# Kernel optimization log

Measured on AMD Instinct MI355X. Metric: run time of the kernel, lower is better.

Reference implementation:

```python
import jax, jax.numpy as jnp
import numpy as np

NUM_USERS = 1_000_000
NUM_AGES = 8
NUM_ATTR = 40
FACE_K = 64
VISUAL_DIM = 2048
HIDDEN = 512
BATCH = 16384
VOCAB = NUM_USERS + 24 + 2 + NUM_AGES + NUM_ATTR  # fm_linear input width


def setup_inputs() -> dict:
    key = jax.random.key(0)
    ks = jax.random.split(key, 24)
    s = 0.02
    inp = {
        "user_id": jax.random.randint(ks[0], (BATCH,), 0, NUM_USERS),
        "hour": jax.random.randint(ks[1], (BATCH,), 0, 24),
        "visual": jax.random.normal(ks[2], (BATCH, VISUAL_DIM), jnp.float32),
        "scale": jax.random.uniform(ks[3], (BATCH, 1), jnp.float32),
        "gender": jax.random.randint(ks[4], (BATCH,), 0, 2),
        "age": jax.random.randint(ks[5], (BATCH,), 0, NUM_AGES),
        "attribute": jax.random.randint(ks[6], (BATCH,), 0, NUM_ATTR),
        # embedding tables
        "user_emb": jax.random.normal(ks[7], (NUM_USERS, FACE_K), jnp.float32) * s,
        "hour_emb": jax.random.normal(ks[8], (24, FACE_K), jnp.float32) * s,
        "gender_emb": jax.random.normal(ks[9], (2, FACE_K), jnp.float32) * s,
        "age_emb": jax.random.normal(ks[10], (NUM_AGES, FACE_K), jnp.float32) * s,
        "attr_emb": jax.random.normal(ks[11], (NUM_ATTR, FACE_K), jnp.float32) * s,
        # visual linear
        "visu_w": jax.random.normal(ks[12], (FACE_K, VISUAL_DIM), jnp.float32) * s,
        "visu_b": jnp.zeros((FACE_K,), jnp.float32),
        # fm linear over concatenated one-hots (width VOCAB, out 2)
        "fm_w": jax.random.normal(ks[13], (2, VOCAB), jnp.float32) * s,
        "fm_b": jnp.zeros((2,), jnp.float32),
        # dnn
        "w1": jax.random.normal(ks[14], (HIDDEN, 6 * FACE_K), jnp.float32) * s,
        "b1": jnp.zeros((HIDDEN,), jnp.float32),
        "w2": jax.random.normal(ks[15], (HIDDEN, HIDDEN), jnp.float32) * s,
        "b2": jnp.zeros((HIDDEN,), jnp.float32),
        "w3": jax.random.normal(ks[16], (2, HIDDEN), jnp.float32) * s,
        "b3": jnp.zeros((2,), jnp.float32),
    }
    return inp


def reference(user_id, hour, visual, scale, gender, age, attribute,
              user_emb, hour_emb, gender_emb, age_emb, attr_emb,
              visu_w, visu_b, fm_w, fm_b, w1, b1, w2, b2, w3, b3):
    B = user_id.shape[0]
    # fm linear: one_hot @ W^T == gather-sum of W columns at the hot indices
    cols = jnp.stack([
        user_id,
        NUM_USERS + hour,
        NUM_USERS + 24 + gender,
        NUM_USERS + 24 + 2 + age,
        NUM_USERS + 24 + 2 + NUM_AGES + attribute,
    ], axis=1)  # [B, 5]
    linear_part = fm_w[:, cols].sum(axis=2).T + fm_b  # [B, 2]

    # embeddings
    user = user_emb[user_id]            # [B, K]
    hr = hour_emb[hour]                 # [B, K]
    face = jnp.stack([gender_emb[gender], attr_emb[attribute], age_emb[age]], axis=1)  # [B,3,K]
    face = scale[:, None, :] * jnp.tanh(face)  # scale [B,1] -> [B,1,1]
    embeddings = jnp.concatenate([user[:, None, :], hr[:, None, :], face], axis=1)  # [B,5,K]

    # FM second order
    so = jnp.square(embeddings.sum(axis=1)) - jnp.square(embeddings).sum(axis=1)  # [B,K]
    second_order = 0.5 * so.sum(axis=1)  # [B]
    fm = linear_part + second_order[:, None]  # [B,2]

    # DNN
    vis = visual @ visu_w.T + visu_b  # [B,K]
    x = jnp.concatenate([embeddings.reshape(B, 5 * FACE_K), vis], axis=1)  # [B,6K]
    x = jax.nn.relu(x @ w1.T + b1)
    x = jax.nn.relu(x @ w2.T + b2)
    x = x @ w3.T + b3
    return jax.nn.softmax(fm + x, axis=1)
```

## Files before the change

### kernel.cpp

```cpp
#include <hip/hip_runtime.h>
#include <hip/hip_bf16.h>
#include <stdint.h>

#define BATCH 16384
#define FACE_K 64
#define VISUAL_DIM 2048
#define HIDDEN 512
#define NUM_USERS 1000000
#define NUM_AGES 8
#define NUM_ATTR 40
#define VOCAB (NUM_USERS + 24 + 2 + NUM_AGES + NUM_ATTR)
#define XDIM 384
#define XS 388
#define HS 516

typedef __bf16 bf16x8 __attribute__((ext_vector_type(8)));
typedef float f32x4 __attribute__((ext_vector_type(4)));

__device__ __forceinline__ uint16_t f2bf(float f) {
    union { float f; uint32_t u; } v; v.f = f;
    uint32_t r = v.u + 0x7fffu + ((v.u >> 16) & 1u);
    return (uint16_t)(r >> 16);
}

__device__ __forceinline__ bf16x8 cvt8(float4 a, float4 b) {
    bf16x8 r;
    r[0] = (__bf16)a.x; r[1] = (__bf16)a.y; r[2] = (__bf16)a.z; r[3] = (__bf16)a.w;
    r[4] = (__bf16)b.x; r[5] = (__bf16)b.y; r[6] = (__bf16)b.z; r[7] = (__bf16)b.w;
    return r;
}

__global__ void cvt_frag(const float* __restrict__ visu_w, const float* __restrict__ w1,
                         const float* __restrict__ w2, uint16_t* __restrict__ vwb,
                         uint16_t* __restrict__ w1b, uint16_t* __restrict__ w2b) {
    int tid = blockIdx.x * blockDim.x + threadIdx.x;
    const float* src;
    uint16_t* dst;
    if (tid < 16384) {
        int lane = tid & 63, fi = tid >> 6;
        int lc = lane & 15, quad = lane >> 4;
        int j = fi & 3, kk = (fi >> 2) & 31, kh = fi >> 7;
        src = visu_w + (size_t)(j * 16 + lc) * VISUAL_DIM + kh * 1024 + kk * 32 + quad * 8;
        dst = vwb + (size_t)tid * 8;
    } else if (tid < 40960) {
        int t2 = tid - 16384;
        int lane = t2 & 63, fi = t2 >> 6;
        int lc = lane & 15, quad = lane >> 4;
        int j = fi & 7, csks = fi >> 3;
        int ks = csks % 12, cs = csks / 12;
        src = w1 + (size_t)(cs * 128 + j * 16 + lc) * XDIM + ks * 32 + quad * 8;
        dst = w1b + (size_t)t2 * 8;
    } else {
        int t3 = tid - 40960;
        int lane = t3 & 63, fi = t3 >> 6;
        int lc = lane & 15, quad = lane >> 4;
        int j = fi & 7, csks = fi >> 3;
        int ks = csks & 15, cs = csks >> 4;
        src = w2 + (size_t)(cs * 128 + j * 16 + lc) * HIDDEN + ks * 32 + quad * 8;
        dst = w2b + (size_t)t3 * 8;
    }
    float4 a = *(const float4*)src;
    float4 b = *(const float4*)(src + 4);
    ushort4 o0, o1;
    o0.x = f2bf(a.x); o0.y = f2bf(a.y); o0.z = f2bf(a.z); o0.w = f2bf(a.w);
    o1.x = f2bf(b.x); o1.y = f2bf(b.y); o1.z = f2bf(b.z); o1.w = f2bf(b.w);
    *(ushort4*)dst = o0;
    *(ushort4*)(dst + 4) = o1;
}

__global__ __launch_bounds__(256) void mega_kernel(
        const int* __restrict__ uid, const int* __restrict__ hour,
        const float* __restrict__ visual, const float* __restrict__ scale,
        const int* __restrict__ gender, const int* __restrict__ age,
        const int* __restrict__ attr,
        const float* __restrict__ user_emb, const float* __restrict__ hour_emb,
        const float* __restrict__ gender_emb, const float* __restrict__ age_emb,
        const float* __restrict__ attr_emb,
        const uint16_t* __restrict__ vwb, const float* __restrict__ visu_b,
        const float* __restrict__ fm_w, const float* __restrict__ fm_b,
        const uint16_t* __restrict__ w1b, const float* __restrict__ b1,
        const uint16_t* __restrict__ w2b, const float* __restrict__ b2,
        const float* __restrict__ w3, const float* __restrict__ b3,
        float* __restrict__ out) {
    __shared__ uint16_t x_tile[32 * XS];
    __shared__ uint16_t h1s[32 * HS];
    __shared__ float red[2][16 * 64];
    __shared__ float fm_s[32][2];
    __shared__ float dred[4][32][2];

    int t = threadIdx.x;
    int wv = t >> 6, lane = t & 63;
    int lc = lane & 15, quad = lane >> 4;
    int m0 = blockIdx.x * 32;

    {
        #pragma unroll 2
        for (int r8 = 0; r8 < 8; ++r8) {
            int row_l = wv * 8 + r8;
            int row_g = m0 + row_l;
            int u = uid[row_g], h = hour[row_g], g = gender[row_g];
            int a = age[row_g], at = attr[row_g];
            float sc = scale[row_g];
            float eu  = user_emb[(size_t)u * 64 + lane];
            float eh  = hour_emb[h * 64 + lane];
            float eg  = sc * tanhf(gender_emb[g * 64 + lane]);
            float eat = sc * tanhf(attr_emb[at * 64 + lane]);
            float eag = sc * tanhf(age_emb[a * 64 + lane]);
            float s  = eu + eh + eg + eat + eag;
            float sq = eu*eu + eh*eh + eg*eg + eat*eat + eag*eag;
            float so = s * s - sq;
            float l0 = 0.f, l1 = 0.f;
            if (lane < 5) {
                int col = (lane == 0) ? u
                        : (lane == 1) ? (NUM_USERS + h)
                        : (lane == 2) ? (NUM_USERS + 24 + g)
                        : (lane == 3) ? (NUM_USERS + 26 + a)
                        :               (NUM_USERS + 34 + at);
                l0 = fm_w[col];
                l1 = fm_w[VOCAB + col];
            }
            for (int m = 32; m; m >>= 1) {
                so += __shfl_xor(so, m);
                l0 += __shfl_xor(l0, m);
                l1 += __shfl_xor(l1, m);
            }
            if (lane == 0) {
                fm_s[row_l][0] = l0 + fm_b[0] + 0.5f * so;
                fm_s[row_l][1] = l1 + fm_b[1] + 0.5f * so;
            }
            int xb = row_l * XS;
            x_tile[xb +       lane] = f2bf(eu);
            x_tile[xb +  64 + lane] = f2bf(eh);
            x_tile[xb + 128 + lane] = f2bf(eg);
            x_tile[xb + 192 + lane] = f2bf(eat);
            x_tile[xb + 256 + lane] = f2bf(eag);
        }
    }

    {
        int rg = wv >> 1, kh = wv & 1;
        const float*    va = visual + (size_t)(m0 + rg * 16 + lc) * VISUAL_DIM + kh * 1024 + quad * 8;
        const uint16_t* vb = vwb + (size_t)(kh * 32 * 4) * 512 + lane * 8;

        f32x4 acc[4];
        #pragma unroll
        for (int j = 0; j < 4; ++j) acc[j] = (f32x4){0.f, 0.f, 0.f, 0.f};

        #pragma unroll 4
        for (int kk = 0; kk < 32; ++kk) {
            float4 a0 = *(const float4*)(va + kk * 32);
            float4 a1 = *(const float4*)(va + kk * 32 + 4);
            bf16x8 af = cvt8(a0, a1);
            #pragma unroll
            for (int j = 0; j < 4; ++j) {
                bf16x8 bf = *(const bf16x8*)(vb + (size_t)(kk * 4 + j) * 512);
                acc[j] = __builtin_amdgcn_mfma_f32_16x16x32_bf16(af, bf, acc[j], 0, 0, 0);
            }
        }
        if (kh == 1) {
            #pragma unroll
            for (int j = 0; j < 4; ++j)
                #pragma unroll
                for (int r = 0; r < 4; ++r)
                    red[rg][(quad * 4 + r) * 64 + j * 16 + lc] = acc[j][r];
        }
        __syncthreads();
        if (kh == 0) {
            #pragma unroll
            for (int j = 0; j < 4; ++j) {
                int col = j * 16 + lc;
                float b = visu_b[col];
                #pragma unroll
                for (int r = 0; r < 4; ++r) {
                    float sum = acc[j][r] + red[rg][(quad * 4 + r) * 64 + col] + b;
                    x_tile[(rg * 16 + quad * 4 + r) * XS + 320 + col] = f2bf(sum);
                }
            }
        }
    }
    __syncthreads();

    {
        int cs = wv;
        const uint16_t* wp1 = w1b + (size_t)(cs * 12 * 8) * 512 + lane * 8;
        const uint16_t* lp0 = x_tile + lc * XS + quad * 8;
        const uint16_t* lp1 = x_tile + (16 + lc) * XS + quad * 8;

        f32x4 acc[2][8];
        #pragma unroll
        for (int i = 0; i < 2; ++i)
            #pragma unroll
            for (int j = 0; j < 8; ++j) acc[i][j] = (f32x4){0.f, 0.f, 0.f, 0.f};

        #pragma unroll 2
        for (int ks = 0; ks < 12; ++ks) {
            union { bf16x8 v; ushort4 h[2]; } u0, u1;
            u0.h[0] = *(const ushort4*)(lp0 + ks * 32);
            u0.h[1] = *(const ushort4*)(lp0 + ks * 32 + 4);
            u1.h[0] = *(const ushort4*)(lp1 + ks * 32);
            u1.h[1] = *(const ushort4*)(lp1 + ks * 32 + 4);
            #pragma unroll
            for (int j = 0; j < 8; ++j) {
                bf16x8 bf = *(const bf16x8*)(wp1 + (size_t)(ks * 8 + j) * 512);
                acc[0][j] = __builtin_amdgcn_mfma_f32_16x16x32_bf16(u0.v, bf, acc[0][j], 0, 0, 0);
                acc[1][j] = __builtin_amdgcn_mfma_f32_16x16x32_bf16(u1.v, bf, acc[1][j], 0, 0, 0);
            }
        }
        #pragma unroll
        for (int j = 0; j < 8; ++j) {
            int col = cs * 128 + j * 16 + lc;
            float bb = b1[col];
            #pragma unroll
            for (int i = 0; i < 2; ++i)
                #pragma unroll
                for (int r = 0; r < 4; ++r) {
                    float v = fmaxf(acc[i][j][r] + bb, 0.f);
                    h1s[(i * 16 + quad * 4 + r) * HS + col] = f2bf(v);
                }
        }
    }
    __syncthreads();

    {
        int cs = wv;
        const uint16_t* wp2 = w2b + (size_t)(cs * 16 * 8) * 512 + lane * 8;
        const uint16_t* lp0 = h1s + lc * HS + quad * 8;
        const uint16_t* lp1 = h1s + (16 + lc) * HS + quad * 8;

        f32x4 acc[2][8];
        #pragma unroll
        for (int i = 0; i < 2; ++i)
            #pragma unroll
            for (int j = 0; j < 8; ++j) acc[i][j] = (f32x4){0.f, 0.f, 0.f, 0.f};

        #pragma unroll 2
        for (int ks = 0; ks < 16; ++ks) {
            union { bf16x8 v; ushort4 h[2]; } u0, u1;
            u0.h[0] = *(const ushort4*)(lp0 + ks * 32);
            u0.h[1] = *(const ushort4*)(lp0 + ks * 32 + 4);
            u1.h[0] = *(const ushort4*)(lp1 + ks * 32);
            u1.h[1] = *(const ushort4*)(lp1 + ks * 32 + 4);
            #pragma unroll
            for (int j = 0; j < 8; ++j) {
                bf16x8 bf = *(const bf16x8*)(wp2 + (size_t)(ks * 8 + j) * 512);
                acc[0][j] = __builtin_amdgcn_mfma_f32_16x16x32_bf16(u0.v, bf, acc[0][j], 0, 0, 0);
                acc[1][j] = __builtin_amdgcn_mfma_f32_16x16x32_bf16(u1.v, bf, acc[1][j], 0, 0, 0);
            }
        }
        float d0[2][4] = {{0,0,0,0},{0,0,0,0}}, d1[2][4] = {{0,0,0,0},{0,0,0,0}};
        #pragma unroll
        for (int j = 0; j < 8; ++j) {
            int col = cs * 128 + j * 16 + lc;
            float bb = b2[col];
            float wa = w3[col], wb = w3[HIDDEN + col];
            #pragma unroll
            for (int i = 0; i < 2; ++i)
                #pragma unroll
                for (int r = 0; r < 4; ++r) {
                    float v = fmaxf(acc[i][j][r] + bb, 0.f);
                    d0[i][r] += v * wa;
                    d1[i][r] += v * wb;
                }
        }
        #pragma unroll
        for (int m = 1; m <= 8; m <<= 1) {
            #pragma unroll
            for (int i = 0; i < 2; ++i)
                #pragma unroll
                for (int r = 0; r < 4; ++r) {
                    d0[i][r] += __shfl_xor(d0[i][r], m);
                    d1[i][r] += __shfl_xor(d1[i][r], m);
                }
        }
        if (lc == 0) {
            #pragma unroll
            for (int i = 0; i < 2; ++i)
                #pragma unroll
                for (int r = 0; r < 4; ++r) {
                    dred[cs][i * 16 + quad * 4 + r][0] = d0[i][r];
                    dred[cs][i * 16 + quad * 4 + r][1] = d1[i][r];
                }
        }
        __syncthreads();
        if (wv == 0 && lc == 0) {
            #pragma unroll
            for (int i = 0; i < 2; ++i)
                #pragma unroll
                for (int r = 0; r < 4; ++r) {
                    int row_l = i * 16 + quad * 4 + r;
                    float l0 = fm_s[row_l][0] + b3[0];
                    float l1 = fm_s[row_l][1] + b3[1];
                    #pragma unroll
                    for (int c = 0; c < 4; ++c) {
                        l0 += dred[c][row_l][0];
                        l1 += dred[c][row_l][1];
                    }
                    float mx = fmaxf(l0, l1);
                    float e0 = __expf(l0 - mx), e1 = __expf(l1 - mx);
                    float inv = 1.f / (e0 + e1);
                    *(float2*)(out + (size_t)(m0 + row_l) * 2) = (float2){e0 * inv, e1 * inv};
                }
        }
    }
}

extern "C" void kernel_launch(void* const* d_in, const int* in_sizes, int n_in,
                              void* d_out, int out_size, void* d_ws, size_t ws_size,
                              hipStream_t stream) {
    const int*   user_id   = (const int*)d_in[0];
    const int*   hour      = (const int*)d_in[1];
    const float* visual    = (const float*)d_in[2];
    const float* scale     = (const float*)d_in[3];
    const int*   gender    = (const int*)d_in[4];
    const int*   age       = (const int*)d_in[5];
    const int*   attribute = (const int*)d_in[6];
    const float* user_emb  = (const float*)d_in[7];
    const float* hour_emb  = (const float*)d_in[8];
    const float* gender_emb= (const float*)d_in[9];
    const float* age_emb   = (const float*)d_in[10];
    const float* attr_emb  = (const float*)d_in[11];
    const float* visu_w    = (const float*)d_in[12];
    const float* visu_b    = (const float*)d_in[13];
    const float* fm_w      = (const float*)d_in[14];
    const float* fm_b      = (const float*)d_in[15];
    const float* w1        = (const float*)d_in[16];
    const float* b1        = (const float*)d_in[17];
    const float* w2        = (const float*)d_in[18];
    const float* b2        = (const float*)d_in[19];
    const float* w3        = (const float*)d_in[20];
    const float* b3        = (const float*)d_in[21];
    float* out = (float*)d_out;

    char* ws = (char*)d_ws;
    uint16_t* vwb = (uint16_t*)ws;
    uint16_t* w1b = vwb + 64 * 2048;
    uint16_t* w2b = w1b + 512 * 384;

    cvt_frag<<<288, 256, 0, stream>>>(visu_w, w1, w2, vwb, w1b, w2b);
    mega_kernel<<<BATCH / 32, 256, 0, stream>>>(
        user_id, hour, visual, scale, gender, age, attribute,
        user_emb, hour_emb, gender_emb, age_emb, attr_emb,
        vwb, visu_b, fm_w, fm_b, w1b, b1, w2b, b2, w3, b3, out);
}
```

Measured before the change: 462.6 us.

## Use 512-thread blocks with 8 waves splitting columns and K, alias shared memory

Doubles the block to 8 waves. Each wave now handles half as many output columns in the two hidden layers and a quarter of K in the visual projection, with a 3-way shared reduction. Shared memory is aliased so h1 reuses the x_tile/red region, which needs an extra barrier before h1 is written. The goal is more waves in flight to hide memory latency on the streamed visual input and fewer accumulator registers per wave. The cost is more cross-wave reduction traffic and extra synchronisation.

```diff
diff --git a/kernel.cpp b/kernel.cpp
--- a/kernel.cpp
+++ b/kernel.cpp
@@ -68,7 +68,7 @@
     *(ushort4*)(dst + 4) = o1;
 }
 
-__global__ __launch_bounds__(256) void mega_kernel(
+__global__ __launch_bounds__(512, 4) void mega_kernel(
         const int* __restrict__ uid, const int* __restrict__ hour,
         const float* __restrict__ visual, const float* __restrict__ scale,
         const int* __restrict__ gender, const int* __restrict__ age,
@@ -82,11 +82,12 @@
         const uint16_t* __restrict__ w2b, const float* __restrict__ b2,
         const float* __restrict__ w3, const float* __restrict__ b3,
         float* __restrict__ out) {
-    __shared__ uint16_t x_tile[32 * XS];
-    __shared__ uint16_t h1s[32 * HS];
-    __shared__ float red[2][16 * 64];
+    __shared__ __align__(16) char smem[49408];
+    uint16_t* x_tile = (uint16_t*)smem;
+    float*    red    = (float*)(smem + 24832);
+    uint16_t* h1s    = (uint16_t*)smem;
     __shared__ float fm_s[32][2];
-    __shared__ float dred[4][32][2];
+    __shared__ float dred[8][32][2];
 
     int t = threadIdx.x;
     int wv = t >> 6, lane = t & 63;
@@ -95,8 +96,8 @@
 
     {
         #pragma unroll 2
-        for (int r8 = 0; r8 < 8; ++r8) {
-            int row_l = wv * 8 + r8;
+        for (int r4 = 0; r4 < 4; ++r4) {
+            int row_l = wv * 4 + r4;
             int row_g = m0 + row_l;
             int u = uid[row_g], h = hour[row_g], g = gender[row_g];
             int a = age[row_g], at = attr[row_g];
@@ -138,16 +139,16 @@
     }
 
     {
-        int rg = wv >> 1, kh = wv & 1;
-        const float*    va = visual + (size_t)(m0 + rg * 16 + lc) * VISUAL_DIM + kh * 1024 + quad * 8;
-        const uint16_t* vb = vwb + (size_t)(kh * 32 * 4) * 512 + lane * 8;
+        int rg = wv & 1, kh = wv >> 1;
+        const float*    va = visual + (size_t)(m0 + rg * 16 + lc) * VISUAL_DIM + kh * 512 + quad * 8;
+        const uint16_t* vb = vwb + (size_t)(kh * 64) * 512 + lane * 8;
 
         f32x4 acc[4];
         #pragma unroll
         for (int j = 0; j < 4; ++j) acc[j] = (f32x4){0.f, 0.f, 0.f, 0.f};
 
         #pragma unroll 4
-        for (int kk = 0; kk < 32; ++kk) {
+        for (int kk = 0; kk < 16; ++kk) {
             float4 a0 = *(const float4*)(va + kk * 32);
             float4 a1 = *(const float4*)(va + kk * 32 + 4);
             bf16x8 af = cvt8(a0, a1);
@@ -157,22 +158,27 @@
                 acc[j] = __builtin_amdgcn_mfma_f32_16x16x32_bf16(af, bf, acc[j], 0, 0, 0);
             }
         }
-        if (kh == 1) {
+        if (kh > 0) {
+            float* base = red + (size_t)(rg * 3 + (kh - 1)) * 1024;
             #pragma unroll
             for (int j = 0; j < 4; ++j)
                 #pragma unroll
                 for (int r = 0; r < 4; ++r)
-                    red[rg][(quad * 4 + r) * 64 + j * 16 + lc] = acc[j][r];
+                    base[(quad * 4 + r) * 64 + j * 16 + lc] = acc[j][r];
         }
         __syncthreads();
         if (kh == 0) {
+            const float* p0 = red + (size_t)(rg * 3 + 0) * 1024;
+            const float* p1 = red + (size_t)(rg * 3 + 1) * 1024;
+            const float* p2 = red + (size_t)(rg * 3 + 2) * 1024;
             #pragma unroll
             for (int j = 0; j < 4; ++j) {
                 int col = j * 16 + lc;
                 float b = visu_b[col];
                 #pragma unroll
                 for (int r = 0; r < 4; ++r) {
-                    float sum = acc[j][r] + red[rg][(quad * 4 + r) * 64 + col] + b;
+                    int e = (quad * 4 + r) * 64 + col;
+                    float sum = acc[j][r] + p0[e] + p1[e] + p2[e] + b;
                     x_tile[(rg * 16 + quad * 4 + r) * XS + 320 + col] = f2bf(sum);
                 }
             }
@@ -182,17 +188,17 @@
 
     {
         int cs = wv;
-        const uint16_t* wp1 = w1b + (size_t)(cs * 12 * 8) * 512 + lane * 8;
+        const uint16_t* wp1 = w1b + (size_t)((cs >> 1) * 96 + (cs & 1) * 4) * 512 + lane * 8;
         const uint16_t* lp0 = x_tile + lc * XS + quad * 8;
         const uint16_t* lp1 = x_tile + (16 + lc) * XS + quad * 8;
 
-        f32x4 acc[2][8];
+        f32x4 acc[2][4];
         #pragma unroll
         for (int i = 0; i < 2; ++i)
             #pragma unroll
-            for (int j = 0; j < 8; ++j) acc[i][j] = (f32x4){0.f, 0.f, 0.f, 0.f};
-
-        #pragma unroll 2
+            for (int j = 0; j < 4; ++j) acc[i][j] = (f32x4){0.f, 0.f, 0.f, 0.f};
+
+        #pragma unroll 3
         for (int ks = 0; ks < 12; ++ks) {
             union { bf16x8 v; ushort4 h[2]; } u0, u1;
             u0.h[0] = *(const ushort4*)(lp0 + ks * 32);
@@ -200,15 +206,16 @@
             u1.h[0] = *(const ushort4*)(lp1 + ks * 32);
             u1.h[1] = *(const ushort4*)(lp1 + ks * 32 + 4);
             #pragma unroll
-            for (int j = 0; j < 8; ++j) {
+            for (int j = 0; j < 4; ++j) {
                 bf16x8 bf = *(const bf16x8*)(wp1 + (size_t)(ks * 8 + j) * 512);
                 acc[0][j] = __builtin_amdgcn_mfma_f32_16x16x32_bf16(u0.v, bf, acc[0][j], 0, 0, 0);
                 acc[1][j] = __builtin_amdgcn_mfma_f32_16x16x32_bf16(u1.v, bf, acc[1][j], 0, 0, 0);
             }
         }
-        #pragma unroll
-        for (int j = 0; j < 8; ++j) {
-            int col = cs * 128 + j * 16 + lc;
+        __syncthreads();
+        #pragma unroll
+        for (int j = 0; j < 4; ++j) {
+            int col = cs * 64 + j * 16 + lc;
             float bb = b1[col];
             #pragma unroll
             for (int i = 0; i < 2; ++i)
@@ -223,17 +230,17 @@
 
     {
         int cs = wv;
-        const uint16_t* wp2 = w2b + (size_t)(cs * 16 * 8) * 512 + lane * 8;
+        const uint16_t* wp2 = w2b + (size_t)((cs >> 1) * 128 + (cs & 1) * 4) * 512 + lane * 8;
         const uint16_t* lp0 = h1s + lc * HS + quad * 8;
         const uint16_t* lp1 = h1s + (16 + lc) * HS + quad * 8;
 
-        f32x4 acc[2][8];
+        f32x4 acc[2][4];
         #pragma unroll
         for (int i = 0; i < 2; ++i)
             #pragma unroll
-            for (int j = 0; j < 8; ++j) acc[i][j] = (f32x4){0.f, 0.f, 0.f, 0.f};
-
-        #pragma unroll 2
+            for (int j = 0; j < 4; ++j) acc[i][j] = (f32x4){0.f, 0.f, 0.f, 0.f};
+
+        #pragma unroll 4
         for (int ks = 0; ks < 16; ++ks) {
             union { bf16x8 v; ushort4 h[2]; } u0, u1;
             u0.h[0] = *(const ushort4*)(lp0 + ks * 32);
@@ -241,7 +248,7 @@
             u1.h[0] = *(const ushort4*)(lp1 + ks * 32);
             u1.h[1] = *(const ushort4*)(lp1 + ks * 32 + 4);
             #pragma unroll
-            for (int j = 0; j < 8; ++j) {
+            for (int j = 0; j < 4; ++j) {
                 bf16x8 bf = *(const bf16x8*)(wp2 + (size_t)(ks * 8 + j) * 512);
                 acc[0][j] = __builtin_amdgcn_mfma_f32_16x16x32_bf16(u0.v, bf, acc[0][j], 0, 0, 0);
                 acc[1][j] = __builtin_amdgcn_mfma_f32_16x16x32_bf16(u1.v, bf, acc[1][j], 0, 0, 0);
@@ -249,8 +256,8 @@
         }
         float d0[2][4] = {{0,0,0,0},{0,0,0,0}}, d1[2][4] = {{0,0,0,0},{0,0,0,0}};
         #pragma unroll
-        for (int j = 0; j < 8; ++j) {
-            int col = cs * 128 + j * 16 + lc;
+        for (int j = 0; j < 4; ++j) {
+            int col = cs * 64 + j * 16 + lc;
             float bb = b2[col];
             float wa = w3[col], wb = w3[HIDDEN + col];
             #pragma unroll
@@ -291,7 +298,7 @@
                     float l0 = fm_s[row_l][0] + b3[0];
                     float l1 = fm_s[row_l][1] + b3[1];
                     #pragma unroll
-                    for (int c = 0; c < 4; ++c) {
+                    for (int c = 0; c < 8; ++c) {
                         l0 += dred[c][row_l][0];
                         l1 += dred[c][row_l][1];
                     }
@@ -337,7 +344,7 @@
     uint16_t* w2b = w1b + 512 * 384;
 
     cvt_frag<<<288, 256, 0, stream>>>(visu_w, w1, w2, vwb, w1b, w2b);
-    mega_kernel<<<BATCH / 32, 256, 0, stream>>>(
+    mega_kernel<<<BATCH / 32, 512, 0, stream>>>(
         user_id, hour, visual, scale, gender, age, attribute,
         user_emb, hour_emb, gender_emb, age_emb, attr_emb,
         vwb, visu_b, fm_w, fm_b, w1b, b1, w2b, b2, w3, b3, out);
```

Result: faster. 438.5 us (-5.2%).
